# Kernel optimization log

Measured on AMD Instinct MI355X. Metric: run time of the kernel, lower is better.

The kernel has to match this reference:

```python
import math
import jax
import jax.numpy as jnp
import numpy as np

B = 64          # graphs per batch
NPG = 1000      # nodes per graph
IN = 64         # input feature dim
H = 128         # hidden dim
DEG = 16        # avg degree
C = 10          # num classes
RATIO = 0.8     # topk ratio
EPS = 1e-5      # batchnorm eps
E = B * NPG * DEG


def setup_inputs() -> dict:
    key = jax.random.key(0)
    ks = jax.random.split(key, 16)
    x = jax.random.normal(ks[0], (B * NPG, IN), jnp.float32)
    # per-graph random edges, then offset to global node ids
    src = jax.random.randint(ks[1], (B, NPG * DEG), 0, NPG)
    dst = jax.random.randint(ks[2], (B, NPG * DEG), 0, NPG)
    off = (jnp.arange(B) * NPG)[:, None]
    edge_index = jnp.stack([(src + off).reshape(-1), (dst + off).reshape(-1)]).astype(jnp.int32)
    batch = jnp.repeat(jnp.arange(B), NPG).astype(jnp.int32)
    edge_weight = jax.random.uniform(ks[3], (E,), jnp.float32)
    # parameters: block 1 conv is [IN,H]; blocks 2-6 are [H,H] (stacked)
    conv1_w = jax.random.normal(ks[4], (IN, H), jnp.float32) * 0.05
    conv_w = jax.random.normal(ks[5], (5, H, H), jnp.float32) * 0.05
    conv_b = jnp.zeros((6, H), jnp.float32)
    bn_gamma = jnp.ones((6, H), jnp.float32)
    bn_beta = jnp.zeros((6, H), jnp.float32)
    bn_mean = jax.random.normal(ks[6], (6, H), jnp.float32) * 0.01
    bn_var = jax.random.uniform(ks[7], (6, H), jnp.float32, 0.5, 1.5)
    pool_w = jax.random.normal(ks[8], (6, H), jnp.float32)
    d1_w = jax.random.normal(ks[9], (2 * H, 4 * H), jnp.float32) * 0.05
    d1_b = jnp.zeros((4 * H,), jnp.float32)
    d2_w = jax.random.normal(ks[10], (4 * H, C), jnp.float32) * 0.05
    d2_b = jnp.zeros((C,), jnp.float32)
    return dict(x=x, edge_index=edge_index, batch=batch, edge_weight=edge_weight,
                conv1_w=conv1_w, conv_w=conv_w, conv_b=conv_b,
                bn_gamma=bn_gamma, bn_beta=bn_beta, bn_mean=bn_mean, bn_var=bn_var,
                pool_w=pool_w, d1_w=d1_w, d1_b=d1_b, d2_w=d2_w, d2_b=d2_b)


def _gcn_conv(h, src, dst, w_e, W, b, n_nodes):
    # PyG GCNConv: add self-loops (weight 1), sym-normalize, aggregate at dst
    xw = h @ W                                        # [N, H]
    deg = jnp.zeros((n_nodes,), h.dtype).at[dst].add(w_e) + 1.0
    dinv = jax.lax.rsqrt(deg)
    coef = dinv[src] * dinv[dst] * w_e                # [E]
    out = jnp.zeros_like(xw).at[dst].add(coef[:, None] * xw[src])
    out = out + (dinv * dinv)[:, None] * xw + b       # self-loop term + bias
    return out


def reference(x, edge_index, batch, edge_weight, conv1_w, conv_w, conv_b,
              bn_gamma, bn_beta, bn_mean, bn_var, pool_w, d1_w, d1_b, d2_w, d2_b):
    src, dst = edge_index[0], edge_index[1]
    w_e = edge_weight
    h = x
    n_cur = NPG
    flats = jnp.zeros((B, 2 * H), x.dtype)
    for i in range(6):
        N = B * n_cur
        W = conv1_w if i == 0 else conv_w[i - 1]
        hc = _gcn_conv(h, src, dst, w_e, W, conv_b[i], N)
        # BatchNorm (inference) + ReLU
        hc = (hc - bn_mean[i]) * (bn_gamma[i] * jax.lax.rsqrt(bn_var[i] + EPS)) + bn_beta[i]
        hc = jax.nn.relu(hc)
        # TopKPooling: score = tanh(x.w/||w||), keep top ceil(ratio*n) per graph
        pw = pool_w[i]
        score = jnp.tanh(hc @ pw / jnp.linalg.norm(pw))   # [N]
        k = math.ceil(RATIO * n_cur)
        vals, idx = jax.lax.top_k(score.reshape(B, n_cur), k)  # [B,k]
        perm = (idx + (jnp.arange(B) * n_cur)[:, None]).reshape(-1)
        h = hc[perm] * vals.reshape(-1, 1)                # [B*k, H]
        # remap/filter edges; dead edges become (0,0) with weight 0
        inv = jnp.full((N,), -1, jnp.int32).at[perm].set(jnp.arange(B * k, dtype=jnp.int32))
        ok = (inv[src] >= 0) & (inv[dst] >= 0)
        src = jnp.where(ok, inv[src], 0)
        dst = jnp.where(ok, inv[dst], 0)
        w_e = jnp.where(ok, w_e, 0.0)
        n_cur = k
        hb = h.reshape(B, k, H)
        flats = flats + jnp.concatenate([hb.mean(axis=1), hb.max(axis=1)], axis=-1)
    # MLP head (dropout is identity in eval)
    hd = jax.nn.relu(flats @ d1_w + d1_b)
    return hd @ d2_w + d2_b
```

## Files before the change

kernel.cpp:

```cpp
#include <hip/hip_runtime.h>
#include <float.h>
#include <math.h>

#define NGR 64
#define NPG0 1000
#define HDIM 128
#define EG 16000
#define NE (NGR*EG)
#define RPS 1008
#define BNEPS 1e-5f
#define POOL_NB 16

typedef short short8 __attribute__((ext_vector_type(8)));
typedef float f4v __attribute__((ext_vector_type(4)));

__global__ __launch_bounds__(256) void k_wsplit(const float* __restrict__ c1w,
    const float* __restrict__ cw, const float* __restrict__ pw,
    unsigned short* __restrict__ wh, unsigned short* __restrict__ wl,
    float* __restrict__ invnorm){
  int l = blockIdx.x, t = threadIdx.x;
  __shared__ float red[2];
  if(t < 128){
    float v = pw[l*HDIM + t];
    float s = v*v;
    #pragma unroll
    for(int o=32;o>0;o>>=1) s += __shfl_down(s, o, 64);
    if((t & 63)==0) red[t>>6] = s;
  }
  __syncthreads();
  if(t==0) invnorm[l] = 1.0f / sqrtf(red[0]+red[1]);
  int K  = (l==0) ? 64 : 128;
  int sh = (l==0) ? 6 : 7;
  const float* src = (l==0) ? c1w : (cw + (size_t)(l-1)*16384);
  int tot = 128*K;
  for(int o=t;o<tot;o+=256){
    int c = o >> sh, k = o & (K-1);
    float f = src[k*128 + c];
    unsigned u  = __float_as_uint(f);
    unsigned uh = (u + 0x7fffu + ((u>>16)&1u)) & 0xffff0000u;
    float r = f - __uint_as_float(uh);
    unsigned v = __float_as_uint(r);
    wh[(size_t)l*16384 + o] = (unsigned short)(uh>>16);
    wl[(size_t)l*16384 + o] = (unsigned short)((v + 0x7fffu + ((v>>16)&1u))>>16);
  }
}

__global__ __launch_bounds__(256) void k_count0(const int* __restrict__ dst,
    const float* __restrict__ we, int* __restrict__ pcnt, float* __restrict__ pdeg){
  int g = blockIdx.x >> 2, sub = blockIdx.x & 3, t = threadIdx.x;
  __shared__ int   cnt[NPG0];
  __shared__ float degl[NPG0];
  for(int i=t;i<NPG0;i+=256){ cnt[i]=0; degl[i]=0.f; }
  __syncthreads();
  int base = g*EG + sub*4000;
  for(int idx=t; idx<4000; idx+=256){
    int e = base + idx;
    int ld = dst[e] - g*NPG0;
    atomicAdd(&cnt[ld], 1);
    atomicAdd(&degl[ld], we[e]);
  }
  __syncthreads();
  int p = blockIdx.x * NPG0;
  for(int i=t;i<NPG0;i+=256){ pcnt[p+i] = cnt[i]; pdeg[p+i] = degl[i]; }
}

__global__ __launch_bounds__(1024) void k_build(const int* __restrict__ pcnt,
    const float* __restrict__ pdeg, const int* __restrict__ src,
    const int* __restrict__ dst, const float* __restrict__ we,
    int* __restrict__ rp, float* __restrict__ dinvz, float* __restrict__ gsc,
    long long* __restrict__ ec){
  int g = blockIdx.x, t = threadIdx.x;
  __shared__ int sc[2][1024];
  __shared__ int cur[NPG0];
  int c = 0;
  if(t < NPG0){
    c = pcnt[(g*4+0)*NPG0+t] + pcnt[(g*4+1)*NPG0+t]
      + pcnt[(g*4+2)*NPG0+t] + pcnt[(g*4+3)*NPG0+t];
    float dg = pdeg[(g*4+0)*NPG0+t] + pdeg[(g*4+1)*NPG0+t]
             + pdeg[(g*4+2)*NPG0+t] + pdeg[(g*4+3)*NPG0+t];
    float dv = 1.0f / sqrtf(dg + 1.0f);
    dinvz[g*NPG0+t] = dv;
    gsc[g*NPG0+t]   = dv;
  }
  sc[0][t] = c;
  __syncthreads();
  int buf = 0;
  for(int d=1; d<1024; d<<=1){
    int v = sc[buf][t];
    if(t>=d) v += sc[buf][t-d];
    sc[buf^1][t] = v;
    __syncthreads();
    buf ^= 1;
  }
  if(t<=NPG0) rp[g*RPS+t] = (t==0) ? 0 : sc[buf][t-1];
  if(t<NPG0)  cur[t]      = (t==0) ? 0 : sc[buf][t-1];
  __syncthreads();
  int base = g*EG;
  for(int idx=t; idx<EG; idx+=1024){
    int e = base + idx;
    int ld = dst[e] - g*NPG0;
    int pos = atomicAdd(&cur[ld], 1);
    ec[(size_t)base + pos] = (((long long)__float_as_int(we[e]))<<32) | (unsigned)src[e];
  }
}

template<int L0>
__global__ __launch_bounds__(256) void k_agg(int n, const int* __restrict__ nlist,
    const int* __restrict__ rp, const long long* __restrict__ ec,
    const float* __restrict__ dinvz, const float* __restrict__ gsc,
    const float* __restrict__ h, float* __restrict__ agg){
  int g = blockIdx.x & 63;
  int chunk = blockIdx.x >> 6;
  int wid = threadIdx.x >> 6, lane = threadIdx.x & 63;
  const int wpg = (gridDim.x >> 6) * 4;
  const int half = lane >> 5, sl32 = lane & 31;
  const int qw   = lane >> 4, sl16 = lane & 15;
  for(int j = chunk*4 + wid; j < n; j += wpg){
    int cg = g*n + j;
    int d  = L0 ? (g*NPG0 + j) : nlist[cg];
    int ld = d - g*NPG0;
    int e0 = rp[g*RPS+ld], e1 = rp[g*RPS+ld+1];
    float dvd = dinvz[d];
    float gsd = gsc[d];
    float4 acc; acc.x=0.f; acc.y=0.f; acc.z=0.f; acc.w=0.f;
    for(int b=e0;b<e1;b+=64){
      int mm = e1-b; if(mm>64) mm=64;
      long long rec = (lane<mm) ? ec[(size_t)g*EG + b + lane] : 0;
      int   sl = (int)(rec & 0xffffffffLL);
      float cl = __int_as_float((int)(rec>>32)) * gsc[sl];
      long long pk = (((long long)__float_as_int(cl))<<32) | (unsigned)sl;
      if(L0){
        int mr = (mm+31) & ~31;
        for(int jj=0;jj<mr;jj+=32){
          #pragma unroll
          for(int u=0;u<8;u++){
            long long p = __shfl(pk, jj + 4*u + qw, 64);
            float c = __int_as_float((int)(p>>32));
            if(c != 0.f){
              int s = (int)(p & 0xffffffffLL);
              float4 hv = *(const float4*)(h + (size_t)s*64 + 4*sl16);
              acc.x += c*hv.x; acc.y += c*hv.y; acc.z += c*hv.z; acc.w += c*hv.w;
            }
          }
        }
      } else {
        int mr = (mm+15) & ~15;
        for(int jj=0;jj<mr;jj+=16){
          #pragma unroll
          for(int u=0;u<8;u++){
            long long p = __shfl(pk, jj + 2*u + half, 64);
            float c = __int_as_float((int)(p>>32));
            if(c != 0.f){
              int s = (int)(p & 0xffffffffLL);
              float4 hv = *(const float4*)(h + (size_t)s*HDIM + 4*sl32);
              acc.x += c*hv.x; acc.y += c*hv.y; acc.z += c*hv.z; acc.w += c*hv.w;
            }
          }
        }
      }
    }
    if(L0){
      acc.x += __shfl_xor(acc.x, 16, 64); acc.y += __shfl_xor(acc.y, 16, 64);
      acc.z += __shfl_xor(acc.z, 16, 64); acc.w += __shfl_xor(acc.w, 16, 64);
      acc.x += __shfl_xor(acc.x, 32, 64); acc.y += __shfl_xor(acc.y, 32, 64);
      acc.z += __shfl_xor(acc.z, 32, 64); acc.w += __shfl_xor(acc.w, 32, 64);
      if(qw==0){
        float4 hs = *(const float4*)(h + (size_t)d*64 + 4*sl16);
        float4 o;
        o.x = dvd*(acc.x + gsd*hs.x); o.y = dvd*(acc.y + gsd*hs.y);
        o.z = dvd*(acc.z + gsd*hs.z); o.w = dvd*(acc.w + gsd*hs.w);
        *(float4*)(agg + (size_t)cg*64 + 4*sl16) = o;
      }
    } else {
      acc.x += __shfl_xor(acc.x, 32, 64); acc.y += __shfl_xor(acc.y, 32, 64);
      acc.z += __shfl_xor(acc.z, 32, 64); acc.w += __shfl_xor(acc.w, 32, 64);
      if(half==0){
        float4 hs = *(const float4*)(h + (size_t)d*HDIM + 4*sl32);
        float4 o;
        o.x = dvd*(acc.x + gsd*hs.x); o.y = dvd*(acc.y + gsd*hs.y);
        o.z = dvd*(acc.z + gsd*hs.z); o.w = dvd*(acc.w + gsd*hs.w);
        *(float4*)(agg + (size_t)cg*HDIM + 4*sl32) = o;
      }
    }
  }
}

__device__ inline void bfsplit(float f, unsigned short &h, unsigned short &l){
  unsigned u  = __float_as_uint(f);
  unsigned uh = (u + 0x7fffu + ((u>>16)&1u)) & 0xffff0000u;
  float r = f - __uint_as_float(uh);
  unsigned v = __float_as_uint(r);
  h = (unsigned short)(uh>>16);
  l = (unsigned short)((v + 0x7fffu + ((v>>16)&1u))>>16);
}

template<int KIN>
__global__ __launch_bounds__(256) void k_gemm_mfma(const float* __restrict__ Ain,
    const unsigned short* __restrict__ Wh, const unsigned short* __restrict__ Wl,
    const float* __restrict__ bias, const float* __restrict__ gamma,
    const float* __restrict__ beta, const float* __restrict__ mean,
    const float* __restrict__ var, const float* __restrict__ pw,
    const float* __restrict__ invn_p, const int* __restrict__ olist,
    float* __restrict__ hout, float* __restrict__ score){
  __shared__ __attribute__((aligned(16))) unsigned short AsH[64*KIN];
  __shared__ __attribute__((aligned(16))) unsigned short AsL[64*KIN];
  __shared__ float sp[64][2];
  int t = threadIdx.x;
  int r0 = blockIdx.x * 64;
  const int lane = t & 63, wid = t >> 6;
  const int wr = wid >> 1, wc = wid & 1;
  const int lr = lane & 15, lq = lane >> 4;

  constexpr int ACH = KIN/4;
  constexpr int ANP = 64*ACH/256;
  #pragma unroll
  for(int p=0;p<ANP;p++){
    int idx = p*256 + t;
    int row = idx / ACH, cq = idx % ACH;
    float4 a = *(const float4*)(Ain + (size_t)(r0+row)*KIN + cq*4);
    ushort4 h4, l4;
    bfsplit(a.x, h4.x, l4.x); bfsplit(a.y, h4.y, l4.y);
    bfsplit(a.z, h4.z, l4.z); bfsplit(a.w, h4.w, l4.w);
    int off = (row*(KIN*2) + cq*8) ^ ((row&7)<<4);
    *(ushort4*)((char*)AsH + off) = h4;
    *(ushort4*)((char*)AsL + off) = l4;
  }
  __syncthreads();

  f4v acc[2][4];
  #pragma unroll
  for(int m=0;m<2;m++)
    #pragma unroll
    for(int n=0;n<4;n++){ acc[m][n][0]=0.f; acc[m][n][1]=0.f; acc[m][n][2]=0.f; acc[m][n][3]=0.f; }

  #pragma unroll
  for(int ks=0; ks<KIN/32; ks++){
    short8 ah[2], al[2], bh[4], bl[4];
    int kb = ks*64 + lq*16;
    int kbs = ks*32 + lq*8;
    #pragma unroll
    for(int n=0;n<4;n++){
      int col = wc*64 + n*16 + lr;
      int goff = col*KIN + kbs;
      bh[n] = *(const short8*)(Wh + goff);
      bl[n] = *(const short8*)(Wl + goff);
    }
    #pragma unroll
    for(int m=0;m<2;m++){
      int row = wr*32 + m*16 + lr;
      int off = (row*(KIN*2) + kb) ^ ((row&7)<<4);
      ah[m] = *(const short8*)((const char*)AsH + off);
      al[m] = *(const short8*)((const char*)AsL + off);
    }
    #pragma unroll
    for(int m=0;m<2;m++){
      #pragma unroll
      for(int n=0;n<4;n++){
        acc[m][n] = __builtin_amdgcn_mfma_f32_16x16x32_bf16(ah[m], bh[n], acc[m][n], 0,0,0);
        acc[m][n] = __builtin_amdgcn_mfma_f32_16x16x32_bf16(ah[m], bl[n], acc[m][n], 0,0,0);
        acc[m][n] = __builtin_amdgcn_mfma_f32_16x16x32_bf16(al[m], bh[n], acc[m][n], 0,0,0);
        acc[m][n] = __builtin_amdgcn_mfma_f32_16x16x32_bf16(al[m], bl[n], acc[m][n], 0,0,0);
      }
    }
  }

  float invn = invn_p[0];
  float bi[4], scv[4], bt[4], mn[4], pv[4];
  #pragma unroll
  for(int n=0;n<4;n++){
    int c = wc*64 + n*16 + lr;
    bi[n]  = bias[c];
    scv[n] = gamma[c] * (1.0f/sqrtf(var[c] + BNEPS));
    bt[n]  = beta[c];
    mn[n]  = mean[c];
    pv[n]  = pw[c];
  }
  #pragma unroll
  for(int m=0;m<2;m++){
    #pragma unroll
    for(int i=0;i<4;i++){
      int rl  = wr*32 + m*16 + lq*4 + i;
      int row = r0 + rl;
      int orig = olist ? olist[row] : row;
      float p = 0.f;
      #pragma unroll
      for(int n=0;n<4;n++){
        float v = fmaxf((acc[m][n][i] + bi[n] - mn[n])*scv[n] + bt[n], 0.f);
        hout[(size_t)orig*HDIM + wc*64 + n*16 + lr] = v;
        p += v*pv[n];
      }
      p += __shfl_xor(p, 1, 64); p += __shfl_xor(p, 2, 64);
      p += __shfl_xor(p, 4, 64); p += __shfl_xor(p, 8, 64);
      if(lr==0) sp[rl][wc] = p;
    }
  }
  __syncthreads();
  if(t < 64) score[r0 + t] = tanhf((sp[t][0] + sp[t][1]) * invn);
}

__global__ __launch_bounds__(512) void k_topk(int n, int k,
    const float* __restrict__ score, const int* __restrict__ curlist,
    float* __restrict__ vals, int* __restrict__ nextlist,
    float* __restrict__ dinvz, float* __restrict__ gsc){
  int g = blockIdx.x, t = threadIdx.x;
  __shared__ unsigned keys[1024];
  __shared__ int hist[256];
  __shared__ int ssum[256];
  __shared__ int sc2[2][512];
  __shared__ int eqbuf[1024];
  __shared__ int eqn;
  __shared__ int sh_B, sh_need, sh_E, sh_cut;
  __shared__ unsigned sh_pref;
  for(int i=t;i<n;i+=512){
    unsigned b = __float_as_uint(score[g*n+i]);
    keys[i] = (b & 0x80000000u) ? ~b : (b | 0x80000000u);
  }
  if(t==0){ sh_need = k; sh_pref = 0u; sh_cut = 0x7fffffff; }
  __syncthreads();
  for(int pass=0; pass<4; pass++){
    int shift = 24 - 8*pass;
    if(t<256) hist[t]=0;
    __syncthreads();
    unsigned pref = sh_pref; int need = sh_need;
    for(int i=t;i<n;i+=512){
      unsigned u = keys[i];
      bool m = (pass==0) || ((u >> (shift+8)) == pref);
      if(m) atomicAdd(&hist[(u>>shift)&255], 1);
    }
    __syncthreads();
    if(t<256) ssum[t] = hist[t];
    __syncthreads();
    for(int d=1; d<256; d<<=1){
      int v=0;
      if(t<256) v = ssum[t] + ((t+d<256)? ssum[t+d] : 0);
      __syncthreads();
      if(t<256) ssum[t] = v;
      __syncthreads();
    }
    if(t<256){
      int Sgt = ssum[t] - hist[t];
      if(Sgt < need && need <= ssum[t]) sh_B = t;
    }
    __syncthreads();
    int B = sh_B;
    if(t==0){
      sh_need = need - (ssum[B] - hist[B]);
      sh_pref = (pass==0) ? (unsigned)B : ((pref<<8) | (unsigned)B);
      if(pass==3) sh_E = hist[B];
    }
    __syncthreads();
  }
  unsigned T = sh_pref; int r_eq = sh_need; int E = sh_E;
  if(E > r_eq){
    if(t==0) eqn = 0;
    __syncthreads();
    for(int i=t;i<n;i+=512) if(keys[i]==T){ int p=atomicAdd(&eqn,1); eqbuf[p]=i; }
    __syncthreads();
    if(t==0){
      int last = -1;
      for(int j=0;j<r_eq;j++){
        int mn = 0x7fffffff;
        for(int q=0;q<E;q++){ int v=eqbuf[q]; if(v>last && v<mn) mn=v; }
        last = mn;
      }
      sh_cut = last;
    }
    __syncthreads();
  }
  int cut = sh_cut;
  int c0=0, c1=0;
  {
    int i=t;
    if(i<n){ unsigned u=keys[i]; c0 = (u>T) || (u==T && i<=cut); }
    i=t+512;
    if(i<n){ unsigned u=keys[i]; c1 = (u>T) || (u==T && i<=cut); }
  }
  sc2[0][t] = c0+c1;
  __syncthreads();
  int buf=0;
  for(int d=1; d<512; d<<=1){
    int v = sc2[buf][t];
    if(t>=d) v += sc2[buf][t-d];
    sc2[buf^1][t]=v;
    __syncthreads();
    buf^=1;
  }
  int base = (t==0) ? 0 : sc2[buf][t-1];
  {
    int i=t;
    if(i<n){
      int orig = curlist ? curlist[g*n+i] : (g*NPG0 + i);
      if(c0){
        unsigned u=keys[i];
        float f = __uint_as_float((u & 0x80000000u) ? (u ^ 0x80000000u) : ~u);
        vals[g*k+base]=f; nextlist[g*k+base]=orig; base++;
      } else { dinvz[orig]=0.f; gsc[orig]=0.f; }
    }
    i=t+512;
    if(i<n){
      int orig = curlist ? curlist[g*n+i] : (g*NPG0 + i);
      if(c1){
        unsigned u=keys[i];
        float f = __uint_as_float((u & 0x80000000u) ? (u ^ 0x80000000u) : ~u);
        vals[g*k+base]=f; nextlist[g*k+base]=orig;
      } else { dinvz[orig]=0.f; gsc[orig]=0.f; }
    }
  }
}

__global__ __launch_bounds__(256) void k_gpd(int k, int do_deg,
    const float* __restrict__ hraw, const float* __restrict__ vals,
    const int* __restrict__ nextlist,
    float* __restrict__ sumst, float* __restrict__ maxst,
    const int* __restrict__ rp, const long long* __restrict__ ec,
    float* __restrict__ dinvz, float* __restrict__ gsc){
  int g = blockIdx.x & 63;
  int chunk = blockIdx.x >> 6;
  int wid = threadIdx.x >> 6, lane = threadIdx.x & 63;
  int ww = chunk*4 + wid;
  const int half = lane >> 5, sl32 = lane & 31;
  const int qw   = lane >> 4, sl16 = lane & 15;
  const int NH = POOL_NB*4*2;
  float4 psum; psum.x=0.f; psum.y=0.f; psum.z=0.f; psum.w=0.f;
  float4 pmax; pmax.x=-FLT_MAX; pmax.y=-FLT_MAX; pmax.z=-FLT_MAX; pmax.w=-FLT_MAX;
  for(int j = ww*2 + half; j < k; j += NH){
    float v = vals[g*k+j];
    int d = nextlist[g*k+j];
    float4 hv = *(const float4*)(hraw + (size_t)d*HDIM + 4*sl32);
    float4 o; o.x=hv.x*v; o.y=hv.y*v; o.z=hv.z*v; o.w=hv.w*v;
    psum.x+=o.x; psum.y+=o.y; psum.z+=o.z; psum.w+=o.w;
    pmax.x=fmaxf(pmax.x,o.x); pmax.y=fmaxf(pmax.y,o.y);
    pmax.z=fmaxf(pmax.z,o.z); pmax.w=fmaxf(pmax.w,o.w);
  }
  if(do_deg){
    const int NQ = POOL_NB*4*4;
    for(int j = ww*4 + qw; j < k; j += NQ){
      int d  = nextlist[g*k + j];
      int ld = d - g*NPG0;
      int e0 = rp[g*RPS+ld], e1 = rp[g*RPS+ld+1];
      float deg = 0.f;
      for(int b=e0+sl16; b<e1; b+=16){
        long long rec = ec[(size_t)g*EG + b];
        int s = (int)(rec & 0xffffffffLL);
        float w = __int_as_float((int)(rec>>32));
        if(dinvz[s] != 0.f) deg += w;
      }
      #pragma unroll
      for(int o=8;o>0;o>>=1) deg += __shfl_xor(deg, o, 64);
      if(sl16==0){
        float dv = 1.0f / sqrtf(deg + 1.0f);
        dinvz[d] = dv;
        gsc[d] = dv * vals[g*k+j];
      }
    }
  }
  psum.x += __shfl_xor(psum.x, 32, 64); psum.y += __shfl_xor(psum.y, 32, 64);
  psum.z += __shfl_xor(psum.z, 32, 64); psum.w += __shfl_xor(psum.w, 32, 64);
  pmax.x = fmaxf(pmax.x, __shfl_xor(pmax.x, 32, 64));
  pmax.y = fmaxf(pmax.y, __shfl_xor(pmax.y, 32, 64));
  pmax.z = fmaxf(pmax.z, __shfl_xor(pmax.z, 32, 64));
  pmax.w = fmaxf(pmax.w, __shfl_xor(pmax.w, 32, 64));
  __shared__ float ss[4][128];
  __shared__ float sm[4][128];
  if(half==0){
    *(float4*)&ss[wid][4*sl32] = psum;
    *(float4*)&sm[wid][4*sl32] = pmax;
  }
  __syncthreads();
  int t = threadIdx.x;
  if(t < 128){
    float s = (ss[0][t]+ss[1][t]) + (ss[2][t]+ss[3][t]);
    float m = fmaxf(fmaxf(sm[0][t], sm[1][t]), fmaxf(sm[2][t], sm[3][t]));
    sumst[(size_t)(chunk*NGR + g)*HDIM + t] = s;
    maxst[(size_t)(chunk*NGR + g)*HDIM + t] = m;
  }
}

__global__ __launch_bounds__(512) void k_head(const float* __restrict__ sumstage,
    const float* __restrict__ maxstage,
    const float* __restrict__ d1w, const float* __restrict__ d1b,
    const float* __restrict__ d2w, const float* __restrict__ d2b, float* __restrict__ out){
  const float kinv[6] = {1.f/800.f, 1.f/640.f, 1.f/512.f, 1.f/410.f, 1.f/328.f, 1.f/263.f};
  int g = blockIdx.x, j = threadIdx.x;
  __shared__ float fl[256];
  __shared__ float hd[512];
  if(j < 128){
    float s = 0.f;
    #pragma unroll
    for(int l=0;l<6;l++){
      float ls = 0.f;
      for(int c=0;c<POOL_NB;c++)
        ls += sumstage[(size_t)((l*POOL_NB + c)*NGR + g)*HDIM + j];
      s += ls * kinv[l];
    }
    fl[j] = s;
  } else if(j < 256){
    int f = j - 128;
    float m = 0.f;
    #pragma unroll
    for(int l=0;l<6;l++){
      float lm = -FLT_MAX;
      for(int c=0;c<POOL_NB;c++)
        lm = fmaxf(lm, maxstage[(size_t)((l*POOL_NB + c)*NGR + g)*HDIM + f]);
      m += lm;
    }
    fl[j] = m;
  }
  __syncthreads();
  float acc = d1b[j];
  for(int i=0;i<256;i++) acc += fl[i]*d1w[i*512+j];
  hd[j] = fmaxf(acc, 0.f);
  __syncthreads();
  if(j < 10){
    float a = d2b[j];
    for(int i=0;i<512;i++) a += hd[i]*d2w[i*10+j];
    out[g*10+j] = a;
  }
}

extern "C" void kernel_launch(void* const* d_in, const int* in_sizes, int n_in,
                              void* d_out, int out_size, void* d_ws, size_t ws_size,
                              hipStream_t stream) {
  const float* x    = (const float*)d_in[0];
  const int* ei     = (const int*)d_in[1];
  const float* ew   = (const float*)d_in[3];
  const float* conv1w = (const float*)d_in[4];
  const float* convw  = (const float*)d_in[5];
  const float* convb  = (const float*)d_in[6];
  const float* bng    = (const float*)d_in[7];
  const float* bnb    = (const float*)d_in[8];
  const float* bnm    = (const float*)d_in[9];
  const float* bnv    = (const float*)d_in[10];
  const float* poolw  = (const float*)d_in[11];
  const float* d1w    = (const float*)d_in[12];
  const float* d1b    = (const float*)d_in[13];
  const float* d2w    = (const float*)d_in[14];
  const float* d2b    = (const float*)d_in[15];
  float* out = (float*)d_out;

  char* w = (char*)d_ws;
  float* horig = (float*)w; w += (size_t)64000*128*4;
  float* hc    = (float*)w; w += (size_t)64000*128*4;
  float* agg0  = (float*)w; w += (size_t)64000*64*4;
  long long* ec = (long long*)w; w += (size_t)NE*8;
  int*   rp    = (int*)w;   w += (size_t)NGR*RPS*4;
  int*   pcnt  = (int*)w;   w += (size_t)256*NPG0*4;
  float* pdeg  = (float*)w; w += (size_t)256*NPG0*4;
  float* dinvz = (float*)w; w += (size_t)64000*4;
  float* gsc   = (float*)w; w += (size_t)64000*4;
  float* score = (float*)w; w += (size_t)64000*4;
  float* vals  = (float*)w; w += (size_t)51200*4;
  int*   listA = (int*)w;   w += (size_t)51200*4;
  int*   listB = (int*)w;   w += (size_t)51200*4;
  float* invno = (float*)w; w += 64;
  float* sumstage = (float*)w; w += (size_t)6*POOL_NB*NGR*HDIM*4;
  float* maxstage = (float*)w; w += (size_t)6*POOL_NB*NGR*HDIM*4;
  unsigned short* whi = (unsigned short*)w; w += (size_t)6*16384*2;
  unsigned short* wlo = (unsigned short*)w; w += (size_t)6*16384*2;

  k_wsplit<<<6,256,0,stream>>>(conv1w, convw, poolw, whi, wlo, invno);

  const int ns[6]={1000,800,640,512,410,328};
  const int ks[6]={800,640,512,410,328,263};

  k_count0<<<256,256,0,stream>>>(ei+NE, ew, pcnt, pdeg);
  k_build<<<64,1024,0,stream>>>(pcnt, pdeg, ei, ei+NE, ew, rp, dinvz, gsc, ec);

  k_agg<1><<<64*32,256,0,stream>>>(1000, nullptr, rp, ec, dinvz, gsc, x, agg0);
  k_gemm_mfma<64><<<1000,256,0,stream>>>(agg0, whi, wlo, convb, bng, bnb, bnm, bnv,
                                         poolw, invno, nullptr, horig, score);
  k_topk<<<64,512,0,stream>>>(1000, 800, score, nullptr, vals, listA, dinvz, gsc);
  k_gpd<<<64*POOL_NB,256,0,stream>>>(800, 1, horig, vals, listA,
                                     sumstage, maxstage, rp, ec, dinvz, gsc);

  int* cur = listA; int* nxt = listB;
  for(int i=1;i<6;i++){
    int n = ns[i], k = ks[i];
    k_agg<0><<<64*32,256,0,stream>>>(n, cur, rp, ec, dinvz, gsc, horig, hc);
    k_gemm_mfma<128><<<n,256,0,stream>>>(hc, whi + (size_t)i*16384, wlo + (size_t)i*16384,
                                         convb+i*128, bng+i*128, bnb+i*128, bnm+i*128,
                                         bnv+i*128, poolw+i*128, invno+i,
                                         cur, horig, score);
    k_topk<<<64,512,0,stream>>>(n, k, score, cur, vals, nxt, dinvz, gsc);
    k_gpd<<<64*POOL_NB,256,0,stream>>>(k, (i<5)?1:0, horig, vals, nxt,
                                       sumstage + (size_t)i*POOL_NB*NGR*HDIM,
                                       maxstage + (size_t)i*POOL_NB*NGR*HDIM,
                                       rp, ec, dinvz, gsc);
    int* tmp = cur; cur = nxt; nxt = tmp;
  }

  k_head<<<64,512,0,stream>>>(sumstage, maxstage, d1w, d1b, d2w, d2b, out);
}
```

Baseline: 520.1 us.

## Repack split weights into k-panels and widen per-lane loads in aggregation

The weight split kernel now stores bf16 hi/lo weights in k-panels of 8 across all 128 columns, so the MFMA B-fragment loads for consecutive columns become contiguous 16-byte reads. The H=128 aggregation path now has each lane handle 8 features (two float4) with four edges processed per wave step, matching the L0 layout. This gives more memory parallelism per gathered row and one shared reduction path. The cost is extra accumulator registers and more shuffle reductions for the non-L0 case.

```diff
diff --git a/kernel.cpp b/kernel.cpp
--- a/kernel.cpp
+++ b/kernel.cpp
@@ -40,8 +40,9 @@
     unsigned uh = (u + 0x7fffu + ((u>>16)&1u)) & 0xffff0000u;
     float r = f - __uint_as_float(uh);
     unsigned v = __float_as_uint(r);
-    wh[(size_t)l*16384 + o] = (unsigned short)(uh>>16);
-    wl[(size_t)l*16384 + o] = (unsigned short)((v + 0x7fffu + ((v>>16)&1u))>>16);
+    int o2 = (k>>3)*1024 + c*8 + (k&7);
+    wh[(size_t)l*16384 + o2] = (unsigned short)(uh>>16);
+    wl[(size_t)l*16384 + o2] = (unsigned short)((v + 0x7fffu + ((v>>16)&1u))>>16);
   }
 }
 
@@ -113,7 +114,6 @@
   int chunk = blockIdx.x >> 6;
   int wid = threadIdx.x >> 6, lane = threadIdx.x & 63;
   const int wpg = (gridDim.x >> 6) * 4;
-  const int half = lane >> 5, sl32 = lane & 31;
   const int qw   = lane >> 4, sl16 = lane & 15;
   for(int j = chunk*4 + wid; j < n; j += wpg){
     int cg = g*n + j;
@@ -122,64 +122,62 @@
     int e0 = rp[g*RPS+ld], e1 = rp[g*RPS+ld+1];
     float dvd = dinvz[d];
     float gsd = gsc[d];
-    float4 acc; acc.x=0.f; acc.y=0.f; acc.z=0.f; acc.w=0.f;
+    float4 a0; a0.x=0.f; a0.y=0.f; a0.z=0.f; a0.w=0.f;
+    float4 a1; a1.x=0.f; a1.y=0.f; a1.z=0.f; a1.w=0.f;
     for(int b=e0;b<e1;b+=64){
       int mm = e1-b; if(mm>64) mm=64;
       long long rec = (lane<mm) ? ec[(size_t)g*EG + b + lane] : 0;
       int   sl = (int)(rec & 0xffffffffLL);
       float cl = __int_as_float((int)(rec>>32)) * gsc[sl];
       long long pk = (((long long)__float_as_int(cl))<<32) | (unsigned)sl;
-      if(L0){
-        int mr = (mm+31) & ~31;
-        for(int jj=0;jj<mr;jj+=32){
-          #pragma unroll
-          for(int u=0;u<8;u++){
-            long long p = __shfl(pk, jj + 4*u + qw, 64);
-            float c = __int_as_float((int)(p>>32));
-            if(c != 0.f){
-              int s = (int)(p & 0xffffffffLL);
+      int mr = (mm+15) & ~15;
+      for(int jj=0;jj<mr;jj+=16){
+        #pragma unroll
+        for(int u=0;u<4;u++){
+          long long p = __shfl(pk, jj + 4*u + qw, 64);
+          float c = __int_as_float((int)(p>>32));
+          if(c != 0.f){
+            int s = (int)(p & 0xffffffffLL);
+            if(L0){
               float4 hv = *(const float4*)(h + (size_t)s*64 + 4*sl16);
-              acc.x += c*hv.x; acc.y += c*hv.y; acc.z += c*hv.z; acc.w += c*hv.w;
+              a0.x += c*hv.x; a0.y += c*hv.y; a0.z += c*hv.z; a0.w += c*hv.w;
+            } else {
+              const float4* hp = (const float4*)(h + (size_t)s*HDIM + 8*sl16);
+              float4 h0 = hp[0], h1 = hp[1];
+              a0.x += c*h0.x; a0.y += c*h0.y; a0.z += c*h0.z; a0.w += c*h0.w;
+              a1.x += c*h1.x; a1.y += c*h1.y; a1.z += c*h1.z; a1.w += c*h1.w;
             }
           }
         }
-      } else {
-        int mr = (mm+15) & ~15;
-        for(int jj=0;jj<mr;jj+=16){
-          #pragma unroll
-          for(int u=0;u<8;u++){
-            long long p = __shfl(pk, jj + 2*u + half, 64);
-            float c = __int_as_float((int)(p>>32));
-            if(c != 0.f){
-              int s = (int)(p & 0xffffffffLL);
-              float4 hv = *(const float4*)(h + (size_t)s*HDIM + 4*sl32);
-              acc.x += c*hv.x; acc.y += c*hv.y; acc.z += c*hv.z; acc.w += c*hv.w;
-            }
-          }
-        }
-      }
-    }
-    if(L0){
-      acc.x += __shfl_xor(acc.x, 16, 64); acc.y += __shfl_xor(acc.y, 16, 64);
-      acc.z += __shfl_xor(acc.z, 16, 64); acc.w += __shfl_xor(acc.w, 16, 64);
-      acc.x += __shfl_xor(acc.x, 32, 64); acc.y += __shfl_xor(acc.y, 32, 64);
-      acc.z += __shfl_xor(acc.z, 32, 64); acc.w += __shfl_xor(acc.w, 32, 64);
-      if(qw==0){
+      }
+    }
+    a0.x += __shfl_xor(a0.x, 16, 64); a0.y += __shfl_xor(a0.y, 16, 64);
+    a0.z += __shfl_xor(a0.z, 16, 64); a0.w += __shfl_xor(a0.w, 16, 64);
+    a0.x += __shfl_xor(a0.x, 32, 64); a0.y += __shfl_xor(a0.y, 32, 64);
+    a0.z += __shfl_xor(a0.z, 32, 64); a0.w += __shfl_xor(a0.w, 32, 64);
+    if(!L0){
+      a1.x += __shfl_xor(a1.x, 16, 64); a1.y += __shfl_xor(a1.y, 16, 64);
+      a1.z += __shfl_xor(a1.z, 16, 64); a1.w += __shfl_xor(a1.w, 16, 64);
+      a1.x += __shfl_xor(a1.x, 32, 64); a1.y += __shfl_xor(a1.y, 32, 64);
+      a1.z += __shfl_xor(a1.z, 32, 64); a1.w += __shfl_xor(a1.w, 32, 64);
+    }
+    if(qw==0){
+      if(L0){
         float4 hs = *(const float4*)(h + (size_t)d*64 + 4*sl16);
         float4 o;
-        o.x = dvd*(acc.x + gsd*hs.x); o.y = dvd*(acc.y + gsd*hs.y);
-        o.z = dvd*(acc.z + gsd*hs.z); o.w = dvd*(acc.w + gsd*hs.w);
+        o.x = dvd*(a0.x + gsd*hs.x); o.y = dvd*(a0.y + gsd*hs.y);
+        o.z = dvd*(a0.z + gsd*hs.z); o.w = dvd*(a0.w + gsd*hs.w);
         *(float4*)(agg + (size_t)cg*64 + 4*sl16) = o;
-      }
-    } else {
-      acc.x += __shfl_xor(acc.x, 32, 64); acc.y += __shfl_xor(acc.y, 32, 64);
-      acc.z += __shfl_xor(acc.z, 32, 64); acc.w += __shfl_xor(acc.w, 32, 64);
-      if(half==0){
-        float4 hs = *(const float4*)(h + (size_t)d*HDIM + 4*sl32);
-        float4 o;
-        o.x = dvd*(acc.x + gsd*hs.x); o.y = dvd*(acc.y + gsd*hs.y);
-        o.z = dvd*(acc.z + gsd*hs.z); o.w = dvd*(acc.w + gsd*hs.w);
-        *(float4*)(agg + (size_t)cg*HDIM + 4*sl32) = o;
+      } else {
+        const float4* hp = (const float4*)(h + (size_t)d*HDIM + 8*sl16);
+        float4 s0 = hp[0], s1 = hp[1];
+        float4 o0, o1;
+        o0.x = dvd*(a0.x + gsd*s0.x); o0.y = dvd*(a0.y + gsd*s0.y);
+        o0.z = dvd*(a0.z + gsd*s0.z); o0.w = dvd*(a0.w + gsd*s0.w);
+        o1.x = dvd*(a1.x + gsd*s1.x); o1.y = dvd*(a1.y + gsd*s1.y);
+        o1.z = dvd*(a1.z + gsd*s1.z); o1.w = dvd*(a1.w + gsd*s1.w);
+        float4* op = (float4*)(agg + (size_t)cg*HDIM + 8*sl16);
+        op[0] = o0; op[1] = o1;
       }
     }
   }
@@ -237,11 +235,11 @@
   for(int ks=0; ks<KIN/32; ks++){
     short8 ah[2], al[2], bh[4], bl[4];
     int kb = ks*64 + lq*16;
-    int kbs = ks*32 + lq*8;
+    int panel = ks*4 + lq;
     #pragma unroll
     for(int n=0;n<4;n++){
       int col = wc*64 + n*16 + lr;
-      int goff = col*KIN + kbs;
+      int goff = (panel*128 + col)*8;
       bh[n] = *(const short8*)(Wh + goff);
       bl[n] = *(const short8*)(Wl + goff);
     }
```

Measured after the change: 484.4 us. 1.07x faster.
